# Optimization experiments

Measured on AMD Instinct MI355X. Metric: run time of the kernel, lower is better.

The kernel has to match this reference:

```python
import jax, jax.numpy as jnp
import numpy as np

B, S, D = 8, 4096, 1024
E = 64            # num_experts
K = 2             # top-k
CAP_F = 1.25      # capacity_factor
TEMP = 0.1        # temperature buffer
Z_COEF = 1e-4
LB_COEF = 1e-4


def setup_inputs() -> dict:
    key = jax.random.key(0)
    kx, k1, k2 = jax.random.split(key, 3)
    x = jax.random.normal(kx, (B, S, D), dtype=jnp.float32)
    W1 = jax.random.normal(k1, (D, D // 2), dtype=jnp.float32) * 0.02
    ln_gamma = jnp.ones((D // 2,), dtype=jnp.float32)
    ln_beta = jnp.zeros((D // 2,), dtype=jnp.float32)
    W2 = jax.random.normal(k2, (D // 2, E), dtype=jnp.float32) * 0.02
    return {"x": x, "W1": W1, "ln_gamma": ln_gamma, "ln_beta": ln_beta, "W2": W2}


def _router_logits(x2, W1, ln_gamma, ln_beta, W2):
    h = x2 @ W1                                   # [T, D//2]
    mu = h.mean(-1, keepdims=True)
    var = h.var(-1, keepdims=True)                # biased var, as torch LayerNorm
    h = (h - mu) / jnp.sqrt(var + 1e-5) * ln_gamma + ln_beta
    h = jax.nn.relu(h)
    logits = h @ W2                               # [T, E]
    logits = jnp.clip(logits, -50.0, 50.0)
    nrm = jnp.linalg.norm(logits, axis=-1, keepdims=True)
    return logits / (jnp.maximum(nrm, 1e-6) + 1e-6)


def reference(x, W1, ln_gamma, ln_beta, W2):
    T = x.shape[0] * x.shape[1]
    x2 = x.reshape(T, -1)
    logits = _router_logits(x2, W1, ln_gamma, ln_beta, W2)   # [T, E]
    routing_weights = jax.nn.softmax(logits / TEMP, axis=-1)

    # top-k + weight renormalization (no_grad in original)
    tw, ti = jax.lax.top_k(routing_weights, K)               # [T, K]
    tw = jnp.clip(tw, 1e-3, 0.8)
    tw = tw / (jnp.maximum(tw.sum(-1, keepdims=True), 1e-6) + 1e-6)
    tw = jax.lax.stop_gradient(tw)
    ti = jax.lax.stop_gradient(ti)

    capacity = CAP_F * T * K / E
    counts = jnp.zeros((E,), dtype=jnp.float32)
    dispatch = jnp.zeros((T, E), dtype=jnp.float32)
    rows = jnp.arange(T)
    for kk in range(K):  # fixed small loop over k, matches sequential scatter semantics
        e = ti[:, kk]                                        # [T] expert ids
        m = counts[e] < capacity                             # capacity check vs pre-step counts
        counts = counts + jax.ops.segment_sum(m.astype(jnp.float32), e, num_segments=E)
        cur = dispatch[rows, e]
        dispatch = dispatch.at[rows, e].set(jnp.where(m, tw[:, kk], cur))

    unrouted = dispatch.sum(-1) == 0                         # [T]
    least_loaded = jnp.argmax(capacity - counts)
    dispatch = jnp.where(unrouted[:, None] & (jnp.arange(E) == least_loaded)[None, :], 1.0, dispatch)
    ndm = dispatch / jnp.maximum(dispatch.sum(-1, keepdims=True), 1e-12)
    ndm = jax.lax.stop_gradient(ndm)

    # training losses
    lp = jnp.clip(jax.nn.log_softmax(logits, axis=-1), -50.0, 50.0)
    z_loss = jnp.minimum(jnp.mean(lp * lp), 100.0)
    usage = ndm.sum(0)
    usage = usage / (jnp.maximum(usage.sum(), 1e-6) + 1e-6)
    usage = jnp.clip(usage, 1e-6, 1.0)
    target = jnp.full((E,), 1.0 / E, dtype=jnp.float32)
    # F.kl_div(log(usage+1e-6), target, reduction='batchmean') on 1-D -> divide by E
    kl = jnp.sum(target * (jnp.log(target) - jnp.log(usage + 1e-6))) / E
    kl = jnp.minimum(kl, 100.0)
    loss = Z_COEF * z_loss + LB_COEF * kl
    loss = jnp.where(jnp.isnan(loss) | jnp.isinf(loss), jnp.float32(0.1), loss)

    return jax.lax.stop_gradient(routing_weights), ndm, loss
```

## Files before the change

### kernel.cpp

```cpp
#include <hip/hip_runtime.h>
#include <hip/hip_bf16.h>
#include <math.h>

#define T_TOK 32768
#define D_IN  1024
#define H_DIM 512
#define N_E   64
#define TM    32
#define BK    16
#define CAPACITY 1280
#define MARGIN   2e-4f
#define MARGIN_F 1e-4f
#define KC1 384

#define WS_H    0ull
#define WS_W1P  67108864ull
#define WS_OFF  69206016ull
#define WS_NEED 69900000ull
#define WS_TI0 0
#define WS_TI1 (4*T_TOK)
#define WS_TW0 (8*T_TOK)
#define WS_TW1 (12*T_TOK)
#define WS_CNT (16*T_TOK)
#define WS_USG (WS_CNT+256)
#define WS_FLAGN (WS_USG+256)
#define WS_ZP  (WS_FLAGN+256)
#define WS_FLAGL (WS_ZP+4096)

typedef __attribute__((ext_vector_type(8))) short short8;
typedef __attribute__((ext_vector_type(4))) float f32x4;

__device__ __forceinline__ float wred64(float v){
#pragma unroll
  for (int m=1;m<64;m<<=1) v += __shfl_xor(v, m, 64);
  return v;
}
__device__ __forceinline__ unsigned short f2bf(float f){
  union { __hip_bfloat16 h; unsigned short u; } cv;
  cv.h = __float2bfloat16(f);
  return cv.u;
}
__device__ __forceinline__ float bf2f(unsigned short u){
  union { __hip_bfloat16 h; unsigned short u; } cv;
  cv.u = u;
  return __bfloat162float(cv.h);
}
__device__ __forceinline__ void cvt8(const float4 A, const float4 B, uint4 &hi, uint4 &lo){
  unsigned h0=f2bf(A.x),h1=f2bf(A.y),h2=f2bf(A.z),h3=f2bf(A.w);
  unsigned h4=f2bf(B.x),h5=f2bf(B.y),h6=f2bf(B.z),h7=f2bf(B.w);
  unsigned l0=f2bf(A.x-bf2f(h0)),l1=f2bf(A.y-bf2f(h1)),l2=f2bf(A.z-bf2f(h2)),l3=f2bf(A.w-bf2f(h3));
  unsigned l4=f2bf(B.x-bf2f(h4)),l5=f2bf(B.y-bf2f(h5)),l6=f2bf(B.z-bf2f(h6)),l7=f2bf(B.w-bf2f(h7));
  hi = make_uint4(h0|(h1<<16), h2|(h3<<16), h4|(h5<<16), h6|(h7<<16));
  lo = make_uint4(l0|(l1<<16), l2|(l3<<16), l4|(l5<<16), l6|(l7<<16));
}

__device__ __forceinline__ float np_sum8acc(const float* a, int n){
  float r0=a[0],r1=a[1],r2=a[2],r3=a[3],r4=a[4],r5=a[5],r6=a[6],r7=a[7];
  int lim = n - (n & 7);
  int i = 8;
  for (; i < lim; i += 8){
    r0=__fadd_rn(r0,a[i]);   r1=__fadd_rn(r1,a[i+1]);
    r2=__fadd_rn(r2,a[i+2]); r3=__fadd_rn(r3,a[i+3]);
    r4=__fadd_rn(r4,a[i+4]); r5=__fadd_rn(r5,a[i+5]);
    r6=__fadd_rn(r6,a[i+6]); r7=__fadd_rn(r7,a[i+7]);
  }
  float res=__fadd_rn(__fadd_rn(__fadd_rn(r0,r1),__fadd_rn(r2,r3)),
                      __fadd_rn(__fadd_rn(r4,r5),__fadd_rn(r6,r7)));
  for (; i < n; ++i) res=__fadd_rn(res,a[i]);
  return res;
}
__device__ __forceinline__ float np_sum512(const float* a){
  float s01=__fadd_rn(np_sum8acc(a,128),     np_sum8acc(a+128,128));
  float s23=__fadd_rn(np_sum8acc(a+256,128), np_sum8acc(a+384,128));
  return __fadd_rn(s01,s23);
}

__global__ void k_pack(const float* __restrict__ W1, unsigned short* __restrict__ W1p)
{
  int T = blockIdx.x*256 + threadIdx.x;
  int lane = T & 63;  int rest = T >> 6;
  int nt = rest & 7;  rest >>= 3;
  int s  = rest & 1;  rest >>= 1;
  int ks = rest & 31; int nb = rest >> 5;
  int n  = nb*128 + nt*16 + (lane & 15);
  int kb = ks*32 + (lane >> 4)*8;
  unsigned short o[8];
#pragma unroll
  for (int j=0;j<8;++j){
    float w = W1[(size_t)(kb+j)*H_DIM + n];
    unsigned short hi = f2bf(w);
    o[j] = s ? f2bf(w - bf2f(hi)) : hi;
  }
  size_t base = ((size_t)((((nb*32+ks)*2+s)*8+nt))*512 + (size_t)lane*8);
#pragma unroll
  for (int j=0;j<8;++j) W1p[base+j] = o[j];
}

__launch_bounds__(256, 2)
__global__ void k_g1(const float* __restrict__ x, const unsigned short* __restrict__ W1p,
                     float* __restrict__ h)
{
  __shared__ __align__(16) unsigned short aF[8192];
  __shared__ __align__(16) unsigned short bF[8192];

  const int b   = blockIdx.x;
  const int nbn = (b >> 3) & 3;
  const int bm  = (b & 7) + (b >> 5) * 8;
  const int t0  = bm * 128;

  const int tid  = threadIdx.x;
  const int lane = tid & 63;
  const int wid  = tid >> 6;
  const int wr4  = (wid >> 1) * 4;
  const int wc4  = (wid & 1) * 4;

  const int s0 = tid, s1 = tid + 256;
  const int row0 = ((s0>>6)<<4) + (s0&15);  const int g0 = (s0>>4)&3;
  const int row1 = ((s1>>6)<<4) + (s1&15);  const int g1 = (s1>>4)&3;
  const size_t xoff0 = (size_t)(t0+row0)*D_IN + g0*8;
  const size_t xoff1 = (size_t)(t0+row1)*D_IN + g1*8;

  f32x4 acc[4][4];
#pragma unroll
  for (int m=0;m<4;++m)
#pragma unroll
    for (int n=0;n<4;++n) acc[m][n] = (f32x4){0.f,0.f,0.f,0.f};

  float4 x0a, x0b, x1a, x1b;
  uint4  bb0, bb1, bb2, bb3;

#define LOADG(KS) do {                                                        \
    int k0_ = (KS)*32;                                                        \
    x0a = *(const float4*)&x[xoff0 + k0_];                                    \
    x0b = *(const float4*)&x[xoff0 + k0_ + 4];                                \
    x1a = *(const float4*)&x[xoff1 + k0_];                                    \
    x1b = *(const float4*)&x[xoff1 + k0_ + 4];                                \
    size_t ch_ = (size_t)(nbn*32 + (KS)) * 8192;                              \
    bb0 = *(const uint4*)&W1p[ch_ + (size_t)(0*256+tid)*8];                   \
    bb1 = *(const uint4*)&W1p[ch_ + (size_t)(1*256+tid)*8];                   \
    bb2 = *(const uint4*)&W1p[ch_ + (size_t)(2*256+tid)*8];                   \
    bb3 = *(const uint4*)&W1p[ch_ + (size_t)(3*256+tid)*8];                   \
  } while(0)

#define WRITE() do {                                                          \
    uint4 hi_, lo_;                                                           \
    cvt8(x0a, x0b, hi_, lo_);                                                 \
    *(uint4*)&aF[s0*8]        = hi_;                                          \
    *(uint4*)&aF[4096 + s0*8] = lo_;                                          \
    cvt8(x1a, x1b, hi_, lo_);                                                 \
    *(uint4*)&aF[s1*8]        = hi_;                                          \
    *(uint4*)&aF[4096 + s1*8] = lo_;                                          \
    *(uint4*)&bF[(0*256+tid)*8] = bb0;                                        \
    *(uint4*)&bF[(1*256+tid)*8] = bb1;                                        \
    *(uint4*)&bF[(2*256+tid)*8] = bb2;                                        \
    *(uint4*)&bF[(3*256+tid)*8] = bb3;                                        \
  } while(0)

  LOADG(0);
  WRITE();
  LOADG(1);
  __syncthreads();

  for (int ks=0; ks<32; ++ks){
    short8 ah[4], al[4], bh4[4], bl4[4];
#pragma unroll
    for (int m=0;m<4;++m){
      ah[m] = *(const short8*)&aF[((wr4+m)*64+lane)*8];
      al[m] = *(const short8*)&aF[4096 + ((wr4+m)*64+lane)*8];
    }
#pragma unroll
    for (int n=0;n<4;++n){
      bh4[n] = *(const short8*)&bF[((wc4+n)*64+lane)*8];
      bl4[n] = *(const short8*)&bF[4096 + ((wc4+n)*64+lane)*8];
    }
#pragma unroll
    for (int m=0;m<4;++m)
#pragma unroll
      for (int n=0;n<4;++n){
        acc[m][n] = __builtin_amdgcn_mfma_f32_16x16x32_bf16(ah[m], bh4[n], acc[m][n], 0,0,0);
        acc[m][n] = __builtin_amdgcn_mfma_f32_16x16x32_bf16(al[m], bh4[n], acc[m][n], 0,0,0);
        acc[m][n] = __builtin_amdgcn_mfma_f32_16x16x32_bf16(ah[m], bl4[n], acc[m][n], 0,0,0);
      }
    __syncthreads();
    if (ks < 31) WRITE();
    if (ks < 30) LOADG(ks+2);
    __syncthreads();
  }
#undef LOADG
#undef WRITE

  const int cr = (lane >> 4) * 4;
  const int cc = lane & 15;
#pragma unroll
  for (int m=0;m<4;++m)
#pragma unroll
    for (int n=0;n<4;++n){
      int row0_ = t0 + (wr4+m)*16 + cr;
      int col   = nbn*128 + (wc4+n)*16 + cc;
#pragma unroll
      for (int r=0;r<4;++r)
        h[(size_t)(row0_+r)*H_DIM + col] = acc[m][n][r];
    }
}

__launch_bounds__(256, 3)
__global__ void k_ln2(const float* __restrict__ h,
                      const float* __restrict__ gamma,
                      const float* __restrict__ beta,
                      const float* __restrict__ W2,
                      float* __restrict__ out_rw,
                      int*   __restrict__ ti0, int* __restrict__ ti1,
                      float* __restrict__ tw0, float* __restrict__ tw1,
                      float* __restrict__ zpart,
                      int* __restrict__ flagn, int* __restrict__ flagl)
{
  __shared__ __align__(16) char smem[53888];
  __shared__ float zw[4];
  float* hnT  = (float*)smem;
  float* redS = (float*)(smem + 36864);
  float* redQ = (float*)(smem + 36864 + 4224);
  float* sW2  = (float*)(smem + 36864);
  float* logitsL = (float*)(smem + 45312);
  float* muA  = (float*)(smem + 53632);
  float* rsA  = (float*)(smem + 53760);

  const int tid  = threadIdx.x;
  const int wv   = tid >> 6;
  const int lane = tid & 63;
  const int tl   = lane & 7;
  const int cl   = lane >> 3;
  const int cbase = wv*128 + cl*16;
  const int t0 = blockIdx.x * TM;

  float acc[4][16];
#pragma unroll
  for (int j=0;j<4;++j)
#pragma unroll
    for (int q=0;q<4;++q)
      *(float4*)&acc[j][q*4] = *(const float4*)&h[(size_t)(t0+tl*4+j)*H_DIM + cbase + q*4];

  const int g = wv*8 + cl;
#pragma unroll
  for (int j=0;j<4;++j) {
    float s=0.f, qq=0.f;
#pragma unroll
    for (int q=0;q<16;++q){ s += acc[j][q]; qq += acc[j][q]*acc[j][q]; }
    redS[(tl*4+j)*33 + g] = s;
    redQ[(tl*4+j)*33 + g] = qq;
  }
  __syncthreads();
  if (tid < 32) {
    float s=0.f, qq=0.f;
    for (int gg=0; gg<32; ++gg){ s += redS[tid*33+gg]; qq += redQ[tid*33+gg]; }
    float mu = s * (1.f/512.f);
    float var = qq * (1.f/512.f) - mu*mu;
    muA[tid] = mu;
    rsA[tid] = rsqrtf(var + 1e-5f);
  }
  __syncthreads();

  {
    float gmv[16], btv[16];
#pragma unroll
    for (int q=0;q<4;++q){
      *(float4*)&gmv[q*4] = *(const float4*)&gamma[cbase+q*4];
      *(float4*)&btv[q*4] = *(const float4*)&beta[cbase+q*4];
    }
    float mu_[4], rs_[4];
#pragma unroll
    for (int j=0;j<4;++j){ mu_[j]=muA[tl*4+j]; rs_[j]=rsA[tl*4+j]; }
#pragma unroll
    for (int j=0;j<4;++j)
#pragma unroll
      for (int q=0;q<16;++q){
        float hv = (acc[j][q]-mu_[j])*rs_[j]*gmv[q] + btv[q];
        acc[j][q] = fmaxf(hv, 0.f);
      }
  }

  float plog[8];
#pragma unroll
  for (int i=0;i<8;++i) plog[i]=0.f;
  const int t2 = tid & 31, e0 = (tid >> 5) * 8;

  for (int p=0; p<2; ++p) {
    if ((wv>>1) == p) {
      int ccb = (wv&1)*128 + cl*16;
#pragma unroll
      for (int j=0;j<4;++j)
#pragma unroll
        for (int q=0;q<16;++q)
          hnT[(ccb+q)*33 + tl*4 + j] = acc[j][q];
    }
    __syncthreads();
    for (int ch=0; ch<8; ++ch) {
      {
        const float4* src = (const float4*)(W2 + (size_t)(p*256+ch*32)*N_E);
        float4* dst = (float4*)sW2;
        dst[tid]     = src[tid];
        dst[tid+256] = src[tid+256];
      }
      __syncthreads();
#pragma unroll
      for (int kk=0; kk<32; ++kk) {
        float hh = hnT[(ch*32+kk)*33 + t2];
        float4 wa = *(const float4*)&sW2[kk*64 + e0];
        float4 wb = *(const float4*)&sW2[kk*64 + e0 + 4];
        plog[0]=fmaf(hh,wa.x,plog[0]); plog[1]=fmaf(hh,wa.y,plog[1]);
        plog[2]=fmaf(hh,wa.z,plog[2]); plog[3]=fmaf(hh,wa.w,plog[3]);
        plog[4]=fmaf(hh,wb.x,plog[4]); plog[5]=fmaf(hh,wb.y,plog[5]);
        plog[6]=fmaf(hh,wb.z,plog[6]); plog[7]=fmaf(hh,wb.w,plog[7]);
      }
      __syncthreads();
    }
  }
#pragma unroll
  for (int i=0;i<8;++i) logitsL[t2*65 + e0 + i] = plog[i];
  __syncthreads();

  const int tE = tid >> 3, jE = tid & 7;
  float v[8];
#pragma unroll
  for (int i=0;i<8;++i){
    float z = logitsL[tE*65 + jE*8 + i];
    v[i] = fminf(fmaxf(z, -50.f), 50.f);
  }
  float ss = 0.f;
#pragma unroll
  for (int i=0;i<8;++i) ss += v[i]*v[i];
#pragma unroll
  for (int m=1;m<8;m<<=1) ss += __shfl_xor(ss, m, 8);
  float scale = 1.f/(fmaxf(sqrtf(ss), 1e-6f) + 1e-6f);
  float ln[8];
#pragma unroll
  for (int i=0;i<8;++i) ln[i] = v[i]*scale;
  float mx = -1e30f;
#pragma unroll
  for (int i=0;i<8;++i) mx = fmaxf(mx, ln[i]);
#pragma unroll
  for (int m=1;m<8;m<<=1) mx = fmaxf(mx, __shfl_xor(mx, m, 8));

  float ex[8], st=0.f, sn=0.f;
#pragma unroll
  for (int i=0;i<8;++i){
    ex[i] = expf((ln[i]-mx)*10.f);
    st += ex[i];
    sn += expf(ln[i]-mx);
  }
#pragma unroll
  for (int m=1;m<8;m<<=1){ st += __shfl_xor(st, m, 8); sn += __shfl_xor(sn, m, 8); }

  float inv_st = 1.f/st;
  float rw[8];
#pragma unroll
  for (int i=0;i<8;++i) rw[i] = ex[i]*inv_st;

  const size_t tok = (size_t)t0 + tE;
  {
    float4* o = (float4*)(out_rw + tok*N_E + jE*8);
    o[0] = make_float4(rw[0],rw[1],rw[2],rw[3]);
    o[1] = make_float4(rw[4],rw[5],rw[6],rw[7]);
  }

  float g1,g2,g3; int i1,i2;
  {
    float bv=-1e30f; int bi=1<<30;
#pragma unroll
    for (int i=0;i<8;++i){ int idx=jE*8+i;
      if (ln[i]>bv || (ln[i]==bv && idx<bi)){ bv=ln[i]; bi=idx; } }
#pragma unroll
    for (int m=1;m<8;m<<=1){ float ov=__shfl_xor(bv,m,8); int oi=__shfl_xor(bi,m,8);
      if (ov>bv || (ov==bv && oi<bi)){ bv=ov; bi=oi; } }
    g1=bv; i1=bi;
    bv=-1e30f; bi=1<<30;
#pragma unroll
    for (int i=0;i<8;++i){ int idx=jE*8+i; if (idx==i1) continue;
      if (ln[i]>bv || (ln[i]==bv && idx<bi)){ bv=ln[i]; bi=idx; } }
#pragma unroll
    for (int m=1;m<8;m<<=1){ float ov=__shfl_xor(bv,m,8); int oi=__shfl_xor(bi,m,8);
      if (ov>bv || (ov==bv && oi<bi)){ bv=ov; bi=oi; } }
    g2=bv; i2=bi;
    bv=-1e30f;
#pragma unroll
    for (int i=0;i<8;++i){ int idx=jE*8+i; if (idx==i1||idx==i2) continue;
      bv = fmaxf(bv, ln[i]); }
#pragma unroll
    for (int m=1;m<8;m<<=1) bv = fmaxf(bv, __shfl_xor(bv,m,8));
    g3=bv;
  }
  if (jE==0){
    float r1 = expf((g1-mx)*10.f)*inv_st;
    float r2 = expf((g2-mx)*10.f)*inv_st;
    float a1 = fminf(fmaxf(r1, 0.001f), 0.8f);
    float a2 = fminf(fmaxf(r2, 0.001f), 0.8f);
    float d  = fmaxf(a1+a2, 1e-6f) + 1e-6f;
    ti0[tok]=i1; ti1[tok]=i2; tw0[tok]=a1/d; tw1[tok]=a2/d;
    if ((g1-g2) < MARGIN_F || (g2-g3) < MARGIN_F){
      int p = atomicAdd(flagn, 1);
      flagl[p] = (int)tok;
    }
  }

  float lse = mx + logf(sn);
  float zq = 0.f;
#pragma unroll
  for (int i=0;i<8;++i){
    float lp = fminf(fmaxf(ln[i]-lse, -50.f), 50.f);
    zq += lp*lp;
  }
  zq = wred64(zq);
  if (lane==0) zw[wv] = zq;
  __syncthreads();
  if (tid==0) zpart[blockIdx.x] = zw[0]+zw[1]+zw[2]+zw[3];
}

__launch_bounds__(256, 3)
__global__ void k_main(const float* __restrict__ x,
                       const float* __restrict__ W1,
                       const float* __restrict__ gamma,
                       const float* __restrict__ beta,
                       const float* __restrict__ W2,
                       float* __restrict__ out_rw,
                       int*   __restrict__ ti0, int* __restrict__ ti1,
                       float* __restrict__ tw0, float* __restrict__ tw1,
                       float* __restrict__ zpart,
                       int* __restrict__ flagn, int* __restrict__ flagl)
{
  __shared__ __align__(16) char smem[53888];
  __shared__ float zw[4];
  float* sW   = (float*)smem;
  float* sX   = (float*)(smem + 32768);
  float* hnT  = (float*)smem;
  float* redS = (float*)(smem + 36864);
  float* redQ = (float*)(smem + 36864 + 4224);
  float* sW2  = (float*)(smem + 36864);
  float* logitsL = (float*)(smem + 45312);
  float* muA  = (float*)(smem + 53632);
  float* rsA  = (float*)(smem + 53760);

  const int tid  = threadIdx.x;
  const int wv   = tid >> 6;
  const int lane = tid & 63;
  const int tl   = lane & 7;
  const int cl   = lane >> 3;
  const int cbase = wv*128 + cl*16;
  const int t0 = blockIdx.x * TM;

  float acc[4][16];
#pragma unroll
  for (int j=0;j<4;++j)
#pragma unroll
    for (int q=0;q<16;++q) acc[j][q]=0.f;

  for (int k0 = 0; k0 < D_IN; k0 += BK) {
    {
      const float4* srcw = (const float4*)(W1 + (size_t)k0 * H_DIM);
      float4* dstw = (float4*)sW;
#pragma unroll
      for (int i=0;i<8;++i) dstw[tid + 256*i] = srcw[tid + 256*i];
    }
    {
      int e0 = tid*2;
      int tt = e0 >> 4, kk = e0 & 15;
      float2 xv = *(const float2*)&x[(size_t)(t0+tt)*D_IN + k0 + kk];
      sX[kk*36 + tt]     = xv.x;
      sX[(kk+1)*36 + tt] = xv.y;
    }
    __syncthreads();
#pragma unroll
    for (int kk=0; kk<BK; ++kk) {
      float4 a = *(const float4*)&sX[kk*36 + tl*4];
      float b[16];
#pragma unroll
      for (int q=0;q<4;++q) *(float4*)&b[q*4] = *(const float4*)&sW[kk*512 + cbase + q*4];
      float av[4] = {a.x, a.y, a.z, a.w};
#pragma unroll
      for (int j=0;j<4;++j)
#pragma unroll
        for (int q=0;q<16;++q)
          acc[j][q] = fmaf(av[j], b[q], acc[j][q]);
    }
    __syncthreads();
  }

  const int g = wv*8 + cl;
#pragma unroll
  for (int j=0;j<4;++j) {
    float s=0.f, qq=0.f;
#pragma unroll
    for (int q=0;q<16;++q){ s += acc[j][q]; qq += acc[j][q]*acc[j][q]; }
    redS[(tl*4+j)*33 + g] = s;
    redQ[(tl*4+j)*33 + g] = qq;
  }
  __syncthreads();
  if (tid < 32) {
    float s=0.f, qq=0.f;
    for (int gg=0; gg<32; ++gg){ s += redS[tid*33+gg]; qq += redQ[tid*33+gg]; }
    float mu = s * (1.f/512.f);
    float var = qq * (1.f/512.f) - mu*mu;
    muA[tid] = mu;
    rsA[tid] = rsqrtf(var + 1e-5f);
  }
  __syncthreads();

  {
    float gmv[16], btv[16];
#pragma unroll
    for (int q=0;q<4;++q){
      *(float4*)&gmv[q*4] = *(const float4*)&gamma[cbase+q*4];
      *(float4*)&btv[q*4] = *(const float4*)&beta[cbase+q*4];
    }
    float mu_[4], rs_[4];
#pragma unroll
    for (int j=0;j<4;++j){ mu_[j]=muA[tl*4+j]; rs_[j]=rsA[tl*4+j]; }
#pragma unroll
    for (int j=0;j<4;++j)
#pragma unroll
      for (int q=0;q<16;++q){
        float hv = (acc[j][q]-mu_[j])*rs_[j]*gmv[q] + btv[q];
        acc[j][q] = fmaxf(hv, 0.f);
      }
  }

  float plog[8];
#pragma unroll
  for (int i=0;i<8;++i) plog[i]=0.f;
  const int t2 = tid & 31, e0 = (tid >> 5) * 8;

  for (int p=0; p<2; ++p) {
    if ((wv>>1) == p) {
      int ccb = (wv&1)*128 + cl*16;
#pragma unroll
      for (int j=0;j<4;++j)
#pragma unroll
        for (int q=0;q<16;++q)
          hnT[(ccb+q)*33 + tl*4 + j] = acc[j][q];
    }
    __syncthreads();
    for (int ch=0; ch<8; ++ch) {
      {
        const float4* src = (const float4*)(W2 + (size_t)(p*256+ch*32)*N_E);
        float4* dst = (float4*)sW2;
        dst[tid]     = src[tid];
        dst[tid+256] = src[tid+256];
      }
      __syncthreads();
#pragma unroll
      for (int kk=0; kk<32; ++kk) {
        float hh = hnT[(ch*32+kk)*33 + t2];
        float4 wa = *(const float4*)&sW2[kk*64 + e0];
        float4 wb = *(const float4*)&sW2[kk*64 + e0 + 4];
        plog[0]=fmaf(hh,wa.x,plog[0]); plog[1]=fmaf(hh,wa.y,plog[1]);
        plog[2]=fmaf(hh,wa.z,plog[2]); plog[3]=fmaf(hh,wa.w,plog[3]);
        plog[4]=fmaf(hh,wb.x,plog[4]); plog[5]=fmaf(hh,wb.y,plog[5]);
        plog[6]=fmaf(hh,wb.z,plog[6]); plog[7]=fmaf(hh,wb.w,plog[7]);
      }
      __syncthreads();
    }
  }
#pragma unroll
  for (int i=0;i<8;++i) logitsL[t2*65 + e0 + i] = plog[i];
  __syncthreads();

  const int tE = tid >> 3, jE = tid & 7;
  float v[8];
#pragma unroll
  for (int i=0;i<8;++i){
    float z = logitsL[tE*65 + jE*8 + i];
    v[i] = fminf(fmaxf(z, -50.f), 50.f);
  }
  float ss = 0.f;
#pragma unroll
  for (int i=0;i<8;++i) ss += v[i]*v[i];
#pragma unroll
  for (int m=1;m<8;m<<=1) ss += __shfl_xor(ss, m, 8);
  float scale = 1.f/(fmaxf(sqrtf(ss), 1e-6f) + 1e-6f);
  float ln[8];
#pragma unroll
  for (int i=0;i<8;++i) ln[i] = v[i]*scale;
  float mx = -1e30f;
#pragma unroll
  for (int i=0;i<8;++i) mx = fmaxf(mx, ln[i]);
#pragma unroll
  for (int m=1;m<8;m<<=1) mx = fmaxf(mx, __shfl_xor(mx, m, 8));

  float ex[8], st=0.f, sn=0.f;
#pragma unroll
  for (int i=0;i<8;++i){
    ex[i] = expf((ln[i]-mx)*10.f);
    st += ex[i];
    sn += expf(ln[i]-mx);
  }
#pragma unroll
  for (int m=1;m<8;m<<=1){ st += __shfl_xor(st, m, 8); sn += __shfl_xor(sn, m, 8); }

  float inv_st = 1.f/st;
  float rw[8];
#pragma unroll
  for (int i=0;i<8;++i) rw[i] = ex[i]*inv_st;

  const size_t tok = (size_t)t0 + tE;
  {
    float4* o = (float4*)(out_rw + tok*N_E + jE*8);
    o[0] = make_float4(rw[0],rw[1],rw[2],rw[3]);
    o[1] = make_float4(rw[4],rw[5],rw[6],rw[7]);
  }

  float g1,g2,g3; int i1,i2;
  {
    float bv=-1e30f; int bi=1<<30;
#pragma unroll
    for (int i=0;i<8;++i){ int idx=jE*8+i;
      if (ln[i]>bv || (ln[i]==bv && idx<bi)){ bv=ln[i]; bi=idx; } }
#pragma unroll
    for (int m=1;m<8;m<<=1){ float ov=__shfl_xor(bv,m,8); int oi=__shfl_xor(bi,m,8);
      if (ov>bv || (ov==bv && oi<bi)){ bv=ov; bi=oi; } }
    g1=bv; i1=bi;
    bv=-1e30f; bi=1<<30;
#pragma unroll
    for (int i=0;i<8;++i){ int idx=jE*8+i; if (idx==i1) continue;
      if (ln[i]>bv || (ln[i]==bv && idx<bi)){ bv=ln[i]; bi=idx; } }
#pragma unroll
    for (int m=1;m<8;m<<=1){ float ov=__shfl_xor(bv,m,8); int oi=__shfl_xor(bi,m,8);
      if (ov>bv || (ov==bv && oi<bi)){ bv=ov; bi=oi; } }
    g2=bv; i2=bi;
    bv=-1e30f;
#pragma unroll
    for (int i=0;i<8;++i){ int idx=jE*8+i; if (idx==i1||idx==i2) continue;
      bv = fmaxf(bv, ln[i]); }
#pragma unroll
    for (int m=1;m<8;m<<=1) bv = fmaxf(bv, __shfl_xor(bv,m,8));
    g3=bv;
  }
  if (jE==0){
    float r1 = expf((g1-mx)*10.f)*inv_st;
    float r2 = expf((g2-mx)*10.f)*inv_st;
    float a1 = fminf(fmaxf(r1, 0.001f), 0.8f);
    float a2 = fminf(fmaxf(r2, 0.001f), 0.8f);
    float d  = fmaxf(a1+a2, 1e-6f) + 1e-6f;
    ti0[tok]=i1; ti1[tok]=i2; tw0[tok]=a1/d; tw1[tok]=a2/d;
    if ((g1-g2) < MARGIN || (g2-g3) < MARGIN){
      int p = atomicAdd(flagn, 1);
      flagl[p] = (int)tok;
    }
  }

  float lse = mx + logf(sn);
  float zq = 0.f;
#pragma unroll
  for (int i=0;i<8;++i){
    float lp = fminf(fmaxf(ln[i]-lse, -50.f), 50.f);
    zq += lp*lp;
  }
  zq = wred64(zq);
  if (lane==0) zw[wv] = zq;
  __syncthreads();
  if (tid==0) zpart[blockIdx.x] = zw[0]+zw[1]+zw[2]+zw[3];
}

__launch_bounds__(256, 1)
__global__ void k_fix(const float* __restrict__ x, const float* __restrict__ W1,
                      const float* __restrict__ gamma, const float* __restrict__ beta,
                      const float* __restrict__ W2,
                      const int* __restrict__ flagl, const int* __restrict__ flagn,
                      int* __restrict__ ti0, int* __restrict__ ti1,
                      float* __restrict__ tw0, float* __restrict__ tw1)
{
  __shared__ __align__(16) float sx[D_IN];
  __shared__ __align__(16) float sW[32*H_DIM];
  __shared__ float hS[H_DIM], sqS[H_DIM], hnS[H_DIM];
  __shared__ float sq64[N_E], eS[N_E];
  __shared__ float sc[4];
  const int tid = threadIdx.x;
  const int nf = *flagn;
  for (int it = blockIdx.x; it < nf; it += gridDim.x) {
    const int tok = flagl[it];
    ((float4*)sx)[tid] = ((const float4*)(x + (size_t)tok*D_IN))[tid];
    const int c0 = tid*2;
    float h0=0.f, h1=0.f, a0=0.f, a1=0.f;
    for (int kb=0; kb<D_IN; kb+=32){
      __syncthreads();
      const float4* src = (const float4*)(W1 + (size_t)kb*H_DIM);
#pragma unroll
      for (int i=0;i<16;++i) ((float4*)sW)[tid + 256*i] = src[tid + 256*i];
      __syncthreads();
#pragma unroll 8
      for (int k=0;k<32;++k){
        float xk = sx[kb+k];
        float2 w = *(const float2*)&sW[k*H_DIM + c0];
        a0 = fmaf(xk, w.x, a0); a1 = fmaf(xk, w.y, a1);
      }
      int ke = kb + 32;
      if (ke == 384){ h0 = a0; h1 = a1; a0 = 0.f; a1 = 0.f; }
      else if (ke == 768 || ke == 1024){
        h0 = __fadd_rn(h0, a0); h1 = __fadd_rn(h1, a1); a0 = 0.f; a1 = 0.f;
      }
    }
    hS[c0]=h0; hS[c0+1]=h1;
    __syncthreads();
    if (tid==0) sc[0] = __fdiv_rn(np_sum512(hS), 512.0f);
    __syncthreads();
    float mu = sc[0];
    float d0 = __fsub_rn(h0, mu), d1 = __fsub_rn(h1, mu);
    sqS[c0]   = __fmul_rn(d0,d0);
    sqS[c0+1] = __fmul_rn(d1,d1);
    __syncthreads();
    if (tid==0){
      float var = __fdiv_rn(np_sum512(sqS), 512.0f);
      sc[1] = __fsqrt_rn(__fadd_rn(var, 1e-5f));
    }
    __syncthreads();
    float den = sc[1];
    float2 gm = *(const float2*)&gamma[c0];
    float2 bt = *(const float2*)&beta[c0];
    hnS[c0]   = fmaxf(__fadd_rn(__fmul_rn(__fdiv_rn(d0,den), gm.x), bt.x), 0.f);
    hnS[c0+1] = fmaxf(__fadd_rn(__fmul_rn(__fdiv_rn(d1,den), gm.y), bt.y), 0.f);
    float b0=0.f, b1=0.f;
    for (int half=0; half<2; ++half){
      __syncthreads();
      const float4* src = (const float4*)(W2 + (size_t)(half*256)*N_E);
#pragma unroll
      for (int i=0;i<16;++i) ((float4*)sW)[tid + 256*i] = src[tid + 256*i];
      __syncthreads();
      if (tid < N_E){
        if (half==0){
#pragma unroll 8
          for (int c=0;c<256;++c) b0 = fmaf(hnS[c], sW[c*N_E+tid], b0);
        } else {
#pragma unroll 8
          for (int c=256;c<KC1;++c) b0 = fmaf(hnS[c], sW[(c-256)*N_E+tid], b0);
#pragma unroll 8
          for (int c=KC1;c<H_DIM;++c) b1 = fmaf(hnS[c], sW[(c-256)*N_E+tid], b1);
        }
      }
    }
    float lgf = 0.f;
    if (tid < N_E){
      lgf = __fadd_rn(b0, b1);
      lgf = fminf(fmaxf(lgf, -50.f), 50.f);
      sq64[tid] = __fmul_rn(lgf, lgf);
    }
    __syncthreads();
    if (tid==0){
      float nrm = __fsqrt_rn(np_sum8acc(sq64, 64));
      sc[2] = __fadd_rn(fmaxf(nrm, 1e-6f), 1e-6f);
    }
    __syncthreads();
    if (tid < N_E){
      float nl = __fdiv_rn(lgf, sc[2]);
      float z  = __fdiv_rn(nl, 0.1f);
      float mz = z;
#pragma unroll
      for (int m=1;m<64;m<<=1) mz = fmaxf(mz, __shfl_xor(mz,m,64));
      eS[tid] = expf(__fsub_rn(z, mz));
    }
    __syncthreads();
    if (tid==0) sc[3] = np_sum8acc(eS, 64);
    __syncthreads();
    if (tid < N_E){
      float rw = __fdiv_rn(eS[tid], sc[3]);
      float bv = rw; int bi = tid;
#pragma unroll
      for (int m=1;m<64;m<<=1){ float ov=__shfl_xor(bv,m,64); int oi=__shfl_xor(bi,m,64);
        if (ov>bv || (ov==bv && oi<bi)){ bv=ov; bi=oi; } }
      float R1=bv; int I1=bi;
      bv = (tid==I1) ? -1.f : rw; bi = (tid==I1) ? (1<<30) : tid;
#pragma unroll
      for (int m=1;m<64;m<<=1){ float ov=__shfl_xor(bv,m,64); int oi=__shfl_xor(bi,m,64);
        if (ov>bv || (ov==bv && oi<bi)){ bv=ov; bi=oi; } }
      float R2=bv; int I2=bi;
      if (tid==0){
        float A1 = fminf(fmaxf(R1, 0.001f), 0.8f);
        float A2 = fminf(fmaxf(R2, 0.001f), 0.8f);
        float dd = __fadd_rn(fmaxf(__fadd_rn(A1,A2), 1e-6f), 1e-6f);
        ti0[tok]=I1; ti1[tok]=I2;
        tw0[tok]=__fdiv_rn(A1,dd); tw1[tok]=__fdiv_rn(A2,dd);
      }
    }
    __syncthreads();
  }
}

__global__ void k_hist(const int* __restrict__ ti0, int* __restrict__ counts)
{
  __shared__ int lh[N_E];
  int tid = threadIdx.x;
  if (tid < N_E) lh[tid] = 0;
  __syncthreads();
  int i = blockIdx.x*256 + tid;
  atomicAdd(&lh[ti0[i]], 1);
  __syncthreads();
  if (tid < N_E) atomicAdd(&counts[tid], lh[tid]);
}

__global__ void k_dispatch(const int* __restrict__ ti0, const int* __restrict__ ti1,
                           const float* __restrict__ tw0, const float* __restrict__ tw1,
                           const int* __restrict__ counts,
                           float* __restrict__ out_ndm, float* __restrict__ usage)
{
  __shared__ float lus[N_E];
  int tid = threadIdx.x;
  if (tid < N_E) lus[tid] = 0.f;
  __syncthreads();
  int gid = blockIdx.x*256 + tid;
  size_t tok = gid >> 3;
  int jE = gid & 7;
  int i0 = ti0[tok], i1 = ti1[tok];
  float w0 = tw0[tok], w1 = tw1[tok];
  float w1m = (counts[i1] < CAPACITY) ? w1 : 0.f;
  float inv = 1.f / fmaxf(w0 + w1m, 1e-12f);
  float vv[8];
#pragma unroll
  for (int i=0;i<8;++i){
    int e = jE*8+i;
    vv[i] = (e==i0) ? w0*inv : (e==i1) ? w1m*inv : 0.f;
  }
  float4* o = (float4*)(out_ndm + tok*N_E + jE*8);
  o[0] = make_float4(vv[0],vv[1],vv[2],vv[3]);
  o[1] = make_float4(vv[4],vv[5],vv[6],vv[7]);
  if (jE==0){
    atomicAdd(&lus[i0], w0*inv);
    atomicAdd(&lus[i1], w1m*inv);
  }
  __syncthreads();
  if (tid < N_E) atomicAdd(&usage[tid], lus[tid]);
}

__global__ void k_final(const float* __restrict__ usage, const float* __restrict__ zpart,
                        float* __restrict__ out_loss)
{
  int e = threadIdx.x;
  float u = usage[e];
  float usum = wred64(u);
  float un = u / (fmaxf(usum, 1e-6f) + 1e-6f);
  un = fminf(fmaxf(un, 1e-6f), 1.0f);
  const float target = 1.0f/64.0f;
  float term = target * (logf(target) - logf(un + 1e-6f));
  float kl = wred64(term) * (1.0f/64.0f);
  kl = fminf(kl, 100.f);
  float zs = 0.f;
  for (int i=e; i<1024; i+=64) zs += zpart[i];
  zs = wred64(zs);
  float z = fminf(zs / (float)(T_TOK*N_E), 100.f);
  float loss = 1e-4f*z + 1e-4f*kl;
  if (isnan(loss) || isinf(loss)) loss = 0.1f;
  if (e==0) out_loss[0] = loss;
}

extern "C" void kernel_launch(void* const* d_in, const int* in_sizes, int n_in,
                              void* d_out, int out_size, void* d_ws, size_t ws_size,
                              hipStream_t stream) {
  const float* x     = (const float*)d_in[0];
  const float* W1    = (const float*)d_in[1];
  const float* gamma = (const float*)d_in[2];
  const float* beta  = (const float*)d_in[3];
  const float* W2    = (const float*)d_in[4];
  float* out = (float*)d_out;

  const bool fast = (ws_size >= WS_NEED);
  char* ws = (char*)d_ws;
  char* sb = ws + (fast ? WS_OFF : 0ull);
  int*   ti0   = (int*)(sb + WS_TI0);
  int*   ti1   = (int*)(sb + WS_TI1);
  float* tw0   = (float*)(sb + WS_TW0);
  float* tw1   = (float*)(sb + WS_TW1);
  int*   cnts  = (int*)(sb + WS_CNT);
  float* usage = (float*)(sb + WS_USG);
  int*   flagn = (int*)(sb + WS_FLAGN);
  float* zpart = (float*)(sb + WS_ZP);
  int*   flagl = (int*)(sb + WS_FLAGL);

  hipMemsetAsync(sb + WS_CNT, 0, 768, stream);

  float* out_rw   = out;
  float* out_ndm  = out + (size_t)T_TOK*N_E;
  float* out_loss = out + 2ull*T_TOK*N_E;

  if (fast) {
    float* hbuf = (float*)(ws + WS_H);
    unsigned short* W1p = (unsigned short*)(ws + WS_W1P);
    k_pack<<<512, 256, 0, stream>>>(W1, W1p);
    k_g1<<<1024, 256, 0, stream>>>(x, W1p, hbuf);
    k_ln2<<<T_TOK/TM, 256, 0, stream>>>(hbuf, gamma, beta, W2,
                                        out_rw, ti0, ti1, tw0, tw1, zpart,
                                        flagn, flagl);
  } else {
    k_main<<<T_TOK/TM, 256, 0, stream>>>(x, W1, gamma, beta, W2,
                                         out_rw, ti0, ti1, tw0, tw1, zpart,
                                         flagn, flagl);
  }
  k_fix<<<1024, 256, 0, stream>>>(x, W1, gamma, beta, W2, flagl, flagn,
                                  ti0, ti1, tw0, tw1);
  k_hist<<<T_TOK/256, 256, 0, stream>>>(ti0, cnts);
  k_dispatch<<<(T_TOK*8)/256, 256, 0, stream>>>(ti0, ti1, tw0, tw1, cnts,
                                                out_ndm, usage);
  k_final<<<1, 64, 0, stream>>>(usage, zpart, out_loss);
}
```

Baseline: 288.7 us.

## Double-buffer GEMM1 LDS tiles and stream W1 directly into LDS

The first GEMM kernel now double-buffers its A and B shared-memory tiles. This lets the next k-step's tile be written while the current one is consumed, so each iteration needs one barrier instead of two. The pre-packed W1 tiles are loaded straight from global memory into LDS with global_load_lds, skipping the register round trip. The cost is twice the LDS footprint (64 KB per block), which may reduce occupancy below the launch-bounds target of 2. The direct-to-LDS loads are asynchronous, and they rely on the single barrier per iteration to be complete before the next k-step reads them.

```diff
diff --git a/kernel.cpp b/kernel.cpp
--- a/kernel.cpp
+++ b/kernel.cpp
@@ -53,6 +53,11 @@
   hi = make_uint4(h0|(h1<<16), h2|(h3<<16), h4|(h5<<16), h6|(h7<<16));
   lo = make_uint4(l0|(l1<<16), l2|(l3<<16), l4|(l5<<16), l6|(l7<<16));
 }
+__device__ __forceinline__ void gload_lds16(const void* g, void* l){
+  __builtin_amdgcn_global_load_lds(
+      (const __attribute__((address_space(1))) unsigned int*)g,
+      (__attribute__((address_space(3))) unsigned int*)l, 16, 0, 0);
+}
 
 __device__ __forceinline__ float np_sum8acc(const float* a, int n){
   float r0=a[0],r1=a[1],r2=a[2],r3=a[3],r4=a[4],r5=a[5],r6=a[6],r7=a[7];
@@ -100,8 +105,8 @@
 __global__ void k_g1(const float* __restrict__ x, const unsigned short* __restrict__ W1p,
                      float* __restrict__ h)
 {
-  __shared__ __align__(16) unsigned short aF[8192];
-  __shared__ __align__(16) unsigned short bF[8192];
+  __shared__ __align__(16) unsigned short aF[2][8192];
+  __shared__ __align__(16) unsigned short bF[2][8192];
 
   const int b   = blockIdx.x;
   const int nbn = (b >> 3) & 3;
@@ -127,51 +132,60 @@
     for (int n=0;n<4;++n) acc[m][n] = (f32x4){0.f,0.f,0.f,0.f};
 
   float4 x0a, x0b, x1a, x1b;
-  uint4  bb0, bb1, bb2, bb3;
-
-#define LOADG(KS) do {                                                        \
+
+#define BISSUE(KS, NB) do {                                                   \
+    size_t ch_ = (size_t)(nbn*32 + (KS)) * 8192;                              \
+    gload_lds16((const void*)&W1p[ch_ + (size_t)(0*256 + wid*64 + lane)*8],   \
+                (void*)&bF[NB][(0*256 + wid*64)*8]);                          \
+    gload_lds16((const void*)&W1p[ch_ + (size_t)(1*256 + wid*64 + lane)*8],   \
+                (void*)&bF[NB][(1*256 + wid*64)*8]);                          \
+    gload_lds16((const void*)&W1p[ch_ + (size_t)(2*256 + wid*64 + lane)*8],   \
+                (void*)&bF[NB][(2*256 + wid*64)*8]);                          \
+    gload_lds16((const void*)&W1p[ch_ + (size_t)(3*256 + wid*64 + lane)*8],   \
+                (void*)&bF[NB][(3*256 + wid*64)*8]);                          \
+  } while(0)
+
+#define LOADA(KS) do {                                                        \
     int k0_ = (KS)*32;                                                        \
     x0a = *(const float4*)&x[xoff0 + k0_];                                    \
     x0b = *(const float4*)&x[xoff0 + k0_ + 4];                                \
     x1a = *(const float4*)&x[xoff1 + k0_];                                    \
     x1b = *(const float4*)&x[xoff1 + k0_ + 4];                                \
-    size_t ch_ = (size_t)(nbn*32 + (KS)) * 8192;                              \
-    bb0 = *(const uint4*)&W1p[ch_ + (size_t)(0*256+tid)*8];                   \
-    bb1 = *(const uint4*)&W1p[ch_ + (size_t)(1*256+tid)*8];                   \
-    bb2 = *(const uint4*)&W1p[ch_ + (size_t)(2*256+tid)*8];                   \
-    bb3 = *(const uint4*)&W1p[ch_ + (size_t)(3*256+tid)*8];                   \
   } while(0)
 
-#define WRITE() do {                                                          \
+#define WRITEA(NB) do {                                                       \
     uint4 hi_, lo_;                                                           \
     cvt8(x0a, x0b, hi_, lo_);                                                 \
-    *(uint4*)&aF[s0*8]        = hi_;                                          \
-    *(uint4*)&aF[4096 + s0*8] = lo_;                                          \
+    *(uint4*)&aF[NB][s0*8]        = hi_;                                      \
+    *(uint4*)&aF[NB][4096 + s0*8] = lo_;                                      \
     cvt8(x1a, x1b, hi_, lo_);                                                 \
-    *(uint4*)&aF[s1*8]        = hi_;                                          \
-    *(uint4*)&aF[4096 + s1*8] = lo_;                                          \
-    *(uint4*)&bF[(0*256+tid)*8] = bb0;                                        \
-    *(uint4*)&bF[(1*256+tid)*8] = bb1;                                        \
-    *(uint4*)&bF[(2*256+tid)*8] = bb2;                                        \
-    *(uint4*)&bF[(3*256+tid)*8] = bb3;                                        \
+    *(uint4*)&aF[NB][s1*8]        = hi_;                                      \
+    *(uint4*)&aF[NB][4096 + s1*8] = lo_;                                      \
   } while(0)
 
-  LOADG(0);
-  WRITE();
-  LOADG(1);
-  __syncthreads();
-
+  BISSUE(0, 0);
+  LOADA(0); WRITEA(0);
+  LOADA(1);
+  __syncthreads();
+
+  int cur = 0;
   for (int ks=0; ks<32; ++ks){
+    if (ks+1 < 32){
+      BISSUE(ks+1, cur^1);
+      WRITEA(cur^1);
+    }
+    if (ks+2 < 32) LOADA(ks+2);
+
     short8 ah[4], al[4], bh4[4], bl4[4];
 #pragma unroll
     for (int m=0;m<4;++m){
-      ah[m] = *(const short8*)&aF[((wr4+m)*64+lane)*8];
-      al[m] = *(const short8*)&aF[4096 + ((wr4+m)*64+lane)*8];
+      ah[m] = *(const short8*)&aF[cur][((wr4+m)*64+lane)*8];
+      al[m] = *(const short8*)&aF[cur][4096 + ((wr4+m)*64+lane)*8];
     }
 #pragma unroll
     for (int n=0;n<4;++n){
-      bh4[n] = *(const short8*)&bF[((wc4+n)*64+lane)*8];
-      bl4[n] = *(const short8*)&bF[4096 + ((wc4+n)*64+lane)*8];
+      bh4[n] = *(const short8*)&bF[cur][((wc4+n)*64+lane)*8];
+      bl4[n] = *(const short8*)&bF[cur][4096 + ((wc4+n)*64+lane)*8];
     }
 #pragma unroll
     for (int m=0;m<4;++m)
@@ -182,12 +196,11 @@
         acc[m][n] = __builtin_amdgcn_mfma_f32_16x16x32_bf16(ah[m], bl4[n], acc[m][n], 0,0,0);
       }
     __syncthreads();
-    if (ks < 31) WRITE();
-    if (ks < 30) LOADG(ks+2);
-    __syncthreads();
-  }
-#undef LOADG
-#undef WRITE
+    cur ^= 1;
+  }
+#undef BISSUE
+#undef LOADA
+#undef WRITEA
 
   const int cr = (lane >> 4) * 4;
   const int cc = lane & 15;
```

New measurement: 298.7 us. +3.5%, slower.
